# Kernel optimization log

Measured on AMD Instinct MI355X. Metric: run time of the kernel, lower is better.

## Reference

```python
import jax, jax.numpy as jnp
import numpy as np

CHUNK = 1024
ROPE_BASE = 10000.0


def _rope_cos_sin(positions, dim, dtype):
    # positions: (nc, C) absolute positions; returns cos/sin of shape (nc, C, dim)
    inv_freq = 1.0 / (ROPE_BASE ** (jnp.arange(0, dim, 2, dtype=jnp.float32) / dim))
    ang = positions.astype(jnp.float32)[..., None] * inv_freq  # (nc, C, dim/2)
    ang = jnp.concatenate([ang, ang], axis=-1)  # rotate-half layout
    return jnp.cos(ang).astype(dtype), jnp.sin(ang).astype(dtype)


def _rotate_half(x):
    x1, x2 = jnp.split(x, 2, axis=-1)
    return jnp.concatenate([-x2, x1], axis=-1)


def setup_inputs() -> dict:
    key = jax.random.key(0)
    kq, kk, kv = jax.random.split(key, 3)
    B, L, H, Dh, Dv = 2, 8192, 16, 64, 64
    return {
        "q": jax.random.normal(kq, (B, L, H, Dh), dtype=jnp.float32),
        "k": jax.random.normal(kk, (B, L, H, Dh), dtype=jnp.float32),
        "v": jax.random.normal(kv, (B, L, H, Dv), dtype=jnp.float32),
        "start_index": 0,
    }


def reference(q, k, v, start_index):
    # Block-diagonal chunked causal attention with inline RoPE, scale = 1.0.
    B, L, H, Dh = q.shape
    Dv = v.shape[-1]
    C = CHUNK
    nc = L // C  # L chosen divisible by chunk_size (pad path is a no-op)

    qc = q.reshape(B, nc, C, H, Dh)
    kc = k.reshape(B, nc, C, H, Dh)
    vc = v.reshape(B, nc, C, H, Dv)

    # Absolute positions per chunk: start_index + chunk_offset + intra-chunk pos
    pos = start_index + jnp.arange(nc)[:, None] * C + jnp.arange(C)[None, :]  # (nc, C)
    cos, sin = _rope_cos_sin(pos, Dh, q.dtype)  # (nc, C, Dh)
    cos = cos[None, :, :, None, :]  # (1, nc, C, 1, Dh)
    sin = sin[None, :, :, None, :]

    q_rot = qc * cos + _rotate_half(qc) * sin
    k_rot = kc * cos + _rotate_half(kc) * sin

    # fp32 scores, NO temperature scaling (scale = 1.0)
    scores = jnp.einsum(
        "bnqhd,bnkhd->bnhqk",
        q_rot.astype(jnp.float32),
        k_rot.astype(jnp.float32),
    )
    causal = jnp.tril(jnp.ones((C, C), dtype=jnp.bool_))
    scores = jnp.where(causal, scores, jnp.finfo(jnp.float32).min)
    attn = jax.nn.softmax(scores, axis=-1)

    out = jnp.einsum("bnhqk,bnkhd->bnqhd", attn, vc.astype(jnp.float32))
    return out.astype(q.dtype).reshape(B, L, H, Dv)
```

## Files before the change

### kernel.cpp

```cpp
#include <hip/hip_runtime.h>
#include <math.h>

typedef _Float16 half8  __attribute__((ext_vector_type(8)));
typedef _Float16 half4  __attribute__((ext_vector_type(4)));
typedef __fp16   f16x2  __attribute__((ext_vector_type(2)));
typedef float    floatx4 __attribute__((ext_vector_type(4)));

#define B_   2
#define L_   8192
#define H_   16
#define D_   64
#define C_   1024
#define NC_  8
#define HD_  1024
#define KSTR 72
#define VSTR 40
#define LOG2B 0.41524101186098314f
#define LOG2E 1.4426950408889634f
#define DTHR  8.0f

__device__ __forceinline__ float fast_exp2(float x) {
#if __has_builtin(__builtin_amdgcn_exp2f)
    return __builtin_amdgcn_exp2f(x);
#else
    return exp2f(x);
#endif
}

__device__ __forceinline__ unsigned pk16(float a, float b) {
    f16x2 r = __builtin_amdgcn_cvt_pkrtz(a, b);
    return __builtin_bit_cast(unsigned, r);
}

__device__ __forceinline__ float rormax16(float v) {
    int x;
    x = __builtin_amdgcn_mov_dpp(__float_as_int(v), 0x121, 0xf, 0xf, true); v = fmaxf(v, __int_as_float(x));
    x = __builtin_amdgcn_mov_dpp(__float_as_int(v), 0x122, 0xf, 0xf, true); v = fmaxf(v, __int_as_float(x));
    x = __builtin_amdgcn_mov_dpp(__float_as_int(v), 0x124, 0xf, 0xf, true); v = fmaxf(v, __int_as_float(x));
    x = __builtin_amdgcn_mov_dpp(__float_as_int(v), 0x128, 0xf, 0xf, true); v = fmaxf(v, __int_as_float(x));
    return v;
}

__global__ __launch_bounds__(256, 2)
void attn_v5(const float* __restrict__ qg, const float* __restrict__ kg,
             const float* __restrict__ vg, const int* __restrict__ sidx,
             float* __restrict__ outg)
{
    __shared__ __align__(16) _Float16 Kl[32 * KSTR];
    __shared__ __align__(16) _Float16 Vt[64 * VSTR];
    __shared__ __align__(16) _Float16 Pt[4][32 * 16];

    const int t  = threadIdx.x;
    const int w  = t >> 6;
    const int lg = (t >> 4) & 3;
    const int ln = t & 15;

    const int bid = blockIdx.x;
    const int j   = bid >> 8;
    const int grp = bid & 255;
    const int h   = grp & 15;
    const int n   = (grp >> 4) & 7;
    const int b   = grp >> 7;

    const int p0   = sidx[0] + n * C_;
    const int qoff = j * 64 + w * 16;

    const long bhbase = ((long)b * L_ + (long)n * C_) * HD_ + (long)h * D_;
    const float* kbase = kg + bhbase;
    const float* vbase = vg + bhbase;

    half8 aq[4][2];
    const int d0 = lg * 8;
    #pragma unroll
    for (int s = 0; s < 4; ++s) {
        const int qr = s * 256 + qoff + ln;
        const float* qp = qg + bhbase + (long)qr * HD_;
        float4 f0 = *(const float4*)(qp + d0);
        float4 f1 = *(const float4*)(qp + d0 + 4);
        float4 g0 = *(const float4*)(qp + d0 + 32);
        float4 g1 = *(const float4*)(qp + d0 + 36);
        float x[8] = {f0.x,f0.y,f0.z,f0.w,f1.x,f1.y,f1.z,f1.w};
        float y[8] = {g0.x,g0.y,g0.z,g0.w,g1.x,g1.y,g1.z,g1.w};
        const float pos = (float)(p0 + qr);
        #pragma unroll
        for (int jj = 0; jj < 8; ++jj) {
            float invf = fast_exp2(-(float)(d0 + jj) * LOG2B);
            float sn, cs; __sincosf(pos * invf, &sn, &cs);
            aq[s][0][jj] = (_Float16)((x[jj] * cs - y[jj] * sn) * LOG2E);
            aq[s][1][jj] = (_Float16)((y[jj] * cs + x[jj] * sn) * LOG2E);
        }
    }

    floatx4 O[4][4];
    floatx4 Ol[4];
    float   mr[4][4];
    #pragma unroll
    for (int s = 0; s < 4; ++s) {
        Ol[s] = (floatx4){0.f,0.f,0.f,0.f};
        #pragma unroll
        for (int dt = 0; dt < 4; ++dt) O[s][dt] = (floatx4){0.f,0.f,0.f,0.f};
        #pragma unroll
        for (int r = 0; r < 4; ++r) mr[s][r] = -1e30f;
    }
    half8 bones;
    #pragma unroll
    for (int jj = 0; jj < 8; ++jj) bones[jj] = (_Float16)1.0f;

    const int sr = t >> 3;
    const int sc = (t & 7) * 4;
    float sinvk[4];
    #pragma unroll
    for (int i = 0; i < 4; ++i) sinvk[i] = fast_exp2(-(float)(sc + i) * LOG2B);
    const int vc = t & 31;
    const int vr = (t >> 5) * 4;

    const int NKT = ((831 + j * 64) >> 5) + 1;
    int nkt_s[4];
    #pragma unroll
    for (int s = 0; s < 4; ++s) nkt_s[s] = ((s * 256 + qoff + 15) >> 5) + 1;

    const unsigned trad = (unsigned)(unsigned long long)(uintptr_t)(&Pt[w][0])
                        + 8u * (unsigned)ln + 256u * (unsigned)lg;

    float4 kp0, kp1; float2 vp0, vp1, vp2, vp3;
    {
        const float* kp = kbase + (long)sr * HD_ + sc;
        kp0 = *(const float4*)kp; kp1 = *(const float4*)(kp + 32);
        const float* vp = vbase + (long)vr * HD_ + 2 * vc;
        vp0 = *(const float2*)vp;           vp1 = *(const float2*)(vp + HD_);
        vp2 = *(const float2*)(vp + 2*HD_); vp3 = *(const float2*)(vp + 3*HD_);
    }

    for (int kt = 0; kt < NKT; ++kt) {
        const int kb0 = kt * 32;
        __syncthreads();
        {
            const float pos = (float)(p0 + kb0 + sr);
            float ka[4] = {kp0.x,kp0.y,kp0.z,kp0.w};
            float kc[4] = {kp1.x,kp1.y,kp1.z,kp1.w};
            half4 o0, o1;
            #pragma unroll
            for (int i = 0; i < 4; ++i) {
                float sn, cs; __sincosf(pos * sinvk[i], &sn, &cs);
                o0[i] = (_Float16)(ka[i] * cs - kc[i] * sn);
                o1[i] = (_Float16)(kc[i] * cs + ka[i] * sn);
            }
            *(half4*)(&Kl[sr * KSTR + sc])      = o0;
            *(half4*)(&Kl[sr * KSTR + sc + 32]) = o1;
            half4 va, vb;
            va[0] = (_Float16)vp0.x; va[1] = (_Float16)vp1.x; va[2] = (_Float16)vp2.x; va[3] = (_Float16)vp3.x;
            vb[0] = (_Float16)vp0.y; vb[1] = (_Float16)vp1.y; vb[2] = (_Float16)vp2.y; vb[3] = (_Float16)vp3.y;
            *(half4*)(&Vt[(2 * vc)     * VSTR + vr]) = va;
            *(half4*)(&Vt[(2 * vc + 1) * VSTR + vr]) = vb;
        }
        if (kt + 1 < NKT) {
            const int kb1 = kb0 + 32;
            const float* kp = kbase + (long)(kb1 + sr) * HD_ + sc;
            kp0 = *(const float4*)kp; kp1 = *(const float4*)(kp + 32);
            const float* vp = vbase + (long)(kb1 + vr) * HD_ + 2 * vc;
            vp0 = *(const float2*)vp;           vp1 = *(const float2*)(vp + HD_);
            vp2 = *(const float2*)(vp + 2*HD_); vp3 = *(const float2*)(vp + 3*HD_);
        }
        __syncthreads();

        half8 bk0[2], bk1[2], bv[4];
        #pragma unroll
        for (int ct = 0; ct < 2; ++ct) {
            const _Float16* kr = &Kl[(ct * 16 + ln) * KSTR + lg * 8];
            bk0[ct] = *(const half8*)kr;
            bk1[ct] = *(const half8*)(kr + 32);
        }
        #pragma unroll
        for (int dt = 0; dt < 4; ++dt)
            bv[dt] = *(const half8*)(&Vt[(dt * 16 + ln) * VSTR + lg * 8]);

        #pragma unroll
        for (int s = 0; s < 4; ++s) {
            if (kt >= nkt_s[s]) continue;
            const int qs = s * 256 + qoff;

            floatx4 sacc[2];
            #pragma unroll
            for (int ct = 0; ct < 2; ++ct) {
                floatx4 acc = (floatx4){0.f,0.f,0.f,0.f};
                acc = __builtin_amdgcn_mfma_f32_16x16x32_f16(aq[s][0], bk0[ct], acc, 0, 0, 0);
                acc = __builtin_amdgcn_mfma_f32_16x16x32_f16(aq[s][1], bk1[ct], acc, 0, 0, 0);
                sacc[ct] = acc;
            }
            if (kb0 + 31 > qs) {
                #pragma unroll
                for (int ct = 0; ct < 2; ++ct) {
                    const int kkc = kb0 + ct * 16 + ln;
                    #pragma unroll
                    for (int r = 0; r < 4; ++r)
                        if (kkc > qs + lg * 4 + r) sacc[ct][r] = -1e30f;
                }
            }

            float tm[4];
            int grow = 0;
            #pragma unroll
            for (int r = 0; r < 4; ++r) {
                tm[r] = rormax16(fmaxf(sacc[0][r], sacc[1][r]));
                grow |= (tm[r] > mr[s][r] + DTHR) ? 1 : 0;
            }
            if (__any(grow)) {
                #pragma unroll
                for (int r = 0; r < 4; ++r) {
                    float mnew  = fmaxf(mr[s][r], tm[r]);
                    float alpha = fast_exp2(mr[s][r] - mnew);
                    mr[s][r] = mnew;
                    Ol[s][r] *= alpha;
                    #pragma unroll
                    for (int dt = 0; dt < 4; ++dt) O[s][dt][r] *= alpha;
                }
            }

            uint2 wa, wb;
            wa.x = pk16(fast_exp2(sacc[0][0] - mr[s][0]), fast_exp2(sacc[0][1] - mr[s][1]));
            wa.y = pk16(fast_exp2(sacc[0][2] - mr[s][2]), fast_exp2(sacc[0][3] - mr[s][3]));
            wb.x = pk16(fast_exp2(sacc[1][0] - mr[s][0]), fast_exp2(sacc[1][1] - mr[s][1]));
            wb.y = pk16(fast_exp2(sacc[1][2] - mr[s][2]), fast_exp2(sacc[1][3] - mr[s][3]));
            *(uint2*)(&Pt[w][ ln       * 16 + lg * 4]) = wa;
            *(uint2*)(&Pt[w][(16 + ln) * 16 + lg * 4]) = wb;
            asm volatile("s_waitcnt lgkmcnt(0)" ::: "memory");
            half4 tlo, thi;
            asm volatile("ds_read_b64_tr_b16 %0, %2\n\t"
                         "ds_read_b64_tr_b16 %1, %2 offset:128"
                         : "=&v"(tlo), "=&v"(thi) : "v"(trad));
            asm volatile("s_waitcnt lgkmcnt(0)" ::: "memory");
            __builtin_amdgcn_sched_barrier(0);
            half8 ap = __builtin_shufflevector(tlo, thi, 0, 1, 2, 3, 4, 5, 6, 7);

            #pragma unroll
            for (int dt = 0; dt < 4; ++dt)
                O[s][dt] = __builtin_amdgcn_mfma_f32_16x16x32_f16(ap, bv[dt], O[s][dt], 0, 0, 0);
            Ol[s] = __builtin_amdgcn_mfma_f32_16x16x32_f16(ap, bones, Ol[s], 0, 0, 0);
        }
    }

    #pragma unroll
    for (int s = 0; s < 4; ++s) {
        const int qs = s * 256 + qoff;
        float inv[4];
        #pragma unroll
        for (int r = 0; r < 4; ++r) inv[r] = 1.0f / Ol[s][r];
        #pragma unroll
        for (int dt = 0; dt < 4; ++dt) {
            #pragma unroll
            for (int r = 0; r < 4; ++r) {
                const int qr = qs + lg * 4 + r;
                outg[bhbase + (long)qr * HD_ + dt * 16 + ln] = O[s][dt][r] * inv[r];
            }
        }
    }
}

extern "C" void kernel_launch(void* const* d_in, const int* in_sizes, int n_in,
                              void* d_out, int out_size, void* d_ws, size_t ws_size,
                              hipStream_t stream) {
    const float* q    = (const float*)d_in[0];
    const float* k    = (const float*)d_in[1];
    const float* v    = (const float*)d_in[2];
    const int*   sidx = (const int*)d_in[3];
    float*       out  = (float*)d_out;

    dim3 grid(B_ * NC_ * H_ * 4);
    dim3 block(256);
    attn_v5<<<grid, block, 0, stream>>>(q, k, v, sidx, out);
}
```

Baseline: 282.9 us.

## Precompute RoPE'd fp16 K and transposed V tiles in workspace prepass

Adds a prep kernel that applies RoPE to K, converts K and V to fp16, and writes them as contiguous 32-row tiles (V transposed) into the workspace. The attention kernel then loads these tiles with single 16-byte loads and stores them to XOR-swizzled shared memory, instead of redoing the sincos rotation and conversion from fp32 for every query block. This removes work repeated across the four query-block CTAs and halves global bytes per tile. In exchange it costs an extra kernel launch and a full workspace write and read pass.

```diff
diff --git a/kernel.cpp b/kernel.cpp
--- a/kernel.cpp
+++ b/kernel.cpp
@@ -13,11 +13,10 @@
 #define C_   1024
 #define NC_  8
 #define HD_  1024
-#define KSTR 72
-#define VSTR 40
 #define LOG2B 0.41524101186098314f
 #define LOG2E 1.4426950408889634f
 #define DTHR  8.0f
+#define NTILE 8192
 
 __device__ __forceinline__ float fast_exp2(float x) {
 #if __has_builtin(__builtin_amdgcn_exp2f)
@@ -42,12 +41,64 @@
 }
 
 __global__ __launch_bounds__(256, 2)
-void attn_v5(const float* __restrict__ qg, const float* __restrict__ kg,
-             const float* __restrict__ vg, const int* __restrict__ sidx,
-             float* __restrict__ outg)
+void prep_v6(const float* __restrict__ kg, const float* __restrict__ vg,
+             const int* __restrict__ sidx, _Float16* __restrict__ ws)
 {
-    __shared__ __align__(16) _Float16 Kl[32 * KSTR];
-    __shared__ __align__(16) _Float16 Vt[64 * VSTR];
+    const int bid = blockIdx.x;
+    const int kt = bid & 31;
+    const int n  = (bid >> 5) & 7;
+    const int h  = (bid >> 8) & 15;
+    const int b  = bid >> 12;
+    const int t  = threadIdx.x;
+
+    const long gk = ((long)b * L_ + (long)n * C_ + (long)kt * 32) * HD_ + (long)h * D_;
+    _Float16* Kt = ws + (long)bid * 2048;
+    _Float16* Vt = ws + (long)NTILE * 2048 + (long)bid * 2048;
+
+    {
+        const int kk = t >> 3;
+        const int sc = (t & 7) * 4;
+        const float pos = (float)(sidx[0] + n * C_ + kt * 32 + kk);
+        const float* kp = kg + gk + (long)kk * HD_ + sc;
+        float4 f0 = *(const float4*)kp;
+        float4 f1 = *(const float4*)(kp + 32);
+        float ka[4] = {f0.x,f0.y,f0.z,f0.w};
+        float kc[4] = {f1.x,f1.y,f1.z,f1.w};
+        half4 o0, o1;
+        #pragma unroll
+        for (int i = 0; i < 4; ++i) {
+            float invf = fast_exp2(-(float)(sc + i) * LOG2B);
+            float sn, cs; __sincosf(pos * invf, &sn, &cs);
+            o0[i] = (_Float16)(ka[i] * cs - kc[i] * sn);
+            o1[i] = (_Float16)(kc[i] * cs + ka[i] * sn);
+        }
+        *(half4*)(Kt + kk * 64 + sc)      = o0;
+        *(half4*)(Kt + kk * 64 + sc + 32) = o1;
+    }
+
+    {
+        const int wv = t >> 6;
+        const int dv = t & 63;
+        const float* vp = vg + gk + (long)(wv * 8) * HD_ + dv;
+        float x[8];
+        #pragma unroll
+        for (int i = 0; i < 8; ++i) x[i] = vp[(long)i * HD_];
+        #pragma unroll
+        for (int q = 0; q < 2; ++q) {
+            half4 pkv;
+            #pragma unroll
+            for (int i = 0; i < 4; ++i) pkv[i] = (_Float16)x[q * 4 + i];
+            *(half4*)(Vt + dv * 32 + wv * 8 + q * 4) = pkv;
+        }
+    }
+}
+
+__global__ __launch_bounds__(256, 2)
+void attn_v6(const float* __restrict__ qg, const int* __restrict__ sidx,
+             const _Float16* __restrict__ ws, float* __restrict__ outg)
+{
+    __shared__ __align__(16) _Float16 KT[2048];
+    __shared__ __align__(16) _Float16 VT[2048];
     __shared__ __align__(16) _Float16 Pt[4][32 * 16];
 
     const int t  = threadIdx.x;
@@ -66,8 +117,9 @@
     const int qoff = j * 64 + w * 16;
 
     const long bhbase = ((long)b * L_ + (long)n * C_) * HD_ + (long)h * D_;
-    const float* kbase = kg + bhbase;
-    const float* vbase = vg + bhbase;
+    const int  tix    = (b * H_ + h) * NC_ + n;
+    const _Float16* ktiles = ws + (long)tix * 32 * 2048;
+    const _Float16* vtiles = ws + (long)NTILE * 2048 + (long)tix * 32 * 2048;
 
     half8 aq[4][2];
     const int d0 = lg * 8;
@@ -106,13 +158,12 @@
     #pragma unroll
     for (int jj = 0; jj < 8; ++jj) bones[jj] = (_Float16)1.0f;
 
-    const int sr = t >> 3;
-    const int sc = (t & 7) * 4;
-    float sinvk[4];
-    #pragma unroll
-    for (int i = 0; i < 4; ++i) sinvk[i] = fast_exp2(-(float)(sc + i) * LOG2B);
-    const int vc = t & 31;
-    const int vr = (t >> 5) * 4;
+    const int skk = t >> 3;
+    const int sdc = (t & 7) * 8;
+    const int svd = t >> 2;
+    const int svk = (t & 3) * 8;
+    const int kwb = skk * 128 + ((sdc * 2) ^ ((skk & 7) << 4));
+    const int vwb = svd * 64  + ((svk * 2) ^ (((svd >> 1) & 3) << 4));
 
     const int NKT = ((831 + j * 64) >> 5) + 1;
     int nkt_s[4];
@@ -122,57 +173,35 @@
     const unsigned trad = (unsigned)(unsigned long long)(uintptr_t)(&Pt[w][0])
                         + 8u * (unsigned)ln + 256u * (unsigned)lg;
 
-    float4 kp0, kp1; float2 vp0, vp1, vp2, vp3;
-    {
-        const float* kp = kbase + (long)sr * HD_ + sc;
-        kp0 = *(const float4*)kp; kp1 = *(const float4*)(kp + 32);
-        const float* vp = vbase + (long)vr * HD_ + 2 * vc;
-        vp0 = *(const float2*)vp;           vp1 = *(const float2*)(vp + HD_);
-        vp2 = *(const float2*)(vp + 2*HD_); vp3 = *(const float2*)(vp + 3*HD_);
-    }
+    half8 kreg = *(const half8*)(ktiles + (long)skk * 64 + sdc);
+    half8 vreg = *(const half8*)(vtiles + (long)svd * 32 + svk);
 
     for (int kt = 0; kt < NKT; ++kt) {
         const int kb0 = kt * 32;
         __syncthreads();
-        {
-            const float pos = (float)(p0 + kb0 + sr);
-            float ka[4] = {kp0.x,kp0.y,kp0.z,kp0.w};
-            float kc[4] = {kp1.x,kp1.y,kp1.z,kp1.w};
-            half4 o0, o1;
-            #pragma unroll
-            for (int i = 0; i < 4; ++i) {
-                float sn, cs; __sincosf(pos * sinvk[i], &sn, &cs);
-                o0[i] = (_Float16)(ka[i] * cs - kc[i] * sn);
-                o1[i] = (_Float16)(kc[i] * cs + ka[i] * sn);
-            }
-            *(half4*)(&Kl[sr * KSTR + sc])      = o0;
-            *(half4*)(&Kl[sr * KSTR + sc + 32]) = o1;
-            half4 va, vb;
-            va[0] = (_Float16)vp0.x; va[1] = (_Float16)vp1.x; va[2] = (_Float16)vp2.x; va[3] = (_Float16)vp3.x;
-            vb[0] = (_Float16)vp0.y; vb[1] = (_Float16)vp1.y; vb[2] = (_Float16)vp2.y; vb[3] = (_Float16)vp3.y;
-            *(half4*)(&Vt[(2 * vc)     * VSTR + vr]) = va;
-            *(half4*)(&Vt[(2 * vc + 1) * VSTR + vr]) = vb;
-        }
+        *(half8*)((char*)KT + kwb) = kreg;
+        *(half8*)((char*)VT + vwb) = vreg;
         if (kt + 1 < NKT) {
-            const int kb1 = kb0 + 32;
-            const float* kp = kbase + (long)(kb1 + sr) * HD_ + sc;
-            kp0 = *(const float4*)kp; kp1 = *(const float4*)(kp + 32);
-            const float* vp = vbase + (long)(kb1 + vr) * HD_ + 2 * vc;
-            vp0 = *(const float2*)vp;           vp1 = *(const float2*)(vp + HD_);
-            vp2 = *(const float2*)(vp + 2*HD_); vp3 = *(const float2*)(vp + 3*HD_);
+            const _Float16* kn = ktiles + (long)(kt + 1) * 2048;
+            const _Float16* vn = vtiles + (long)(kt + 1) * 2048;
+            kreg = *(const half8*)(kn + (long)skk * 64 + sdc);
+            vreg = *(const half8*)(vn + (long)svd * 32 + svk);
         }
         __syncthreads();
 
         half8 bk0[2], bk1[2], bv[4];
         #pragma unroll
         for (int ct = 0; ct < 2; ++ct) {
-            const _Float16* kr = &Kl[(ct * 16 + ln) * KSTR + lg * 8];
-            bk0[ct] = *(const half8*)kr;
-            bk1[ct] = *(const half8*)(kr + 32);
-        }
-        #pragma unroll
-        for (int dt = 0; dt < 4; ++dt)
-            bv[dt] = *(const half8*)(&Vt[(dt * 16 + ln) * VSTR + lg * 8]);
+            const int row = ct * 16 + ln;
+            const char* base = (const char*)KT + row * 128;
+            bk0[ct] = *(const half8*)(base + ((lg * 16)      ^ ((row & 7) << 4)));
+            bk1[ct] = *(const half8*)(base + ((64 + lg * 16) ^ ((row & 7) << 4)));
+        }
+        #pragma unroll
+        for (int dt = 0; dt < 4; ++dt) {
+            const int dv = dt * 16 + ln;
+            bv[dt] = *(const half8*)((const char*)VT + dv * 64 + ((lg * 16) ^ (((dv >> 1) & 3) << 4)));
+        }
 
         #pragma unroll
         for (int s = 0; s < 4; ++s) {
@@ -264,8 +293,9 @@
     const float* v    = (const float*)d_in[2];
     const int*   sidx = (const int*)d_in[3];
     float*       out  = (float*)d_out;
-
-    dim3 grid(B_ * NC_ * H_ * 4);
+    _Float16*    ws   = (_Float16*)d_ws;
+
     dim3 block(256);
-    attn_v5<<<grid, block, 0, stream>>>(q, k, v, sidx, out);
-}
+    prep_v6<<<dim3(NTILE), block, 0, stream>>>(k, v, sidx, ws);
+    attn_v6<<<dim3(B_ * NC_ * H_ * 4), block, 0, stream>>>(q, sidx, ws, out);
+}
```

After: 322.3 us. 1.14x slower.
